# Kernel optimization log

Measured on AMD Instinct MI355X. Metric: run time of the kernel, lower is better.

The kernel has to match this reference:

```python
import jax, jax.numpy as jnp
import numpy as np
from jax import lax

B, T, I, H, L, C = 128, 784, 1, 256, 20, 10  # batch, seq_len, input, hidden, layers, classes


def setup_inputs() -> dict:
    key = jax.random.key(0)
    ks = jax.random.split(key, 9)
    s = 1.0 / np.sqrt(H)  # torch nn.RNN init: U(-1/sqrt(H), 1/sqrt(H))
    u = lambda k, shape: jax.random.uniform(k, shape, jnp.float32, -s, s)
    return {
        "x": jax.random.normal(ks[0], (B, T, I), jnp.float32),
        "W_ih0": u(ks[1], (H, I)),        # layer 0 input proj
        "b_ih0": u(ks[2], (H,)),
        "W_ih": u(ks[3], (L - 1, H, H)),  # layers 1..L-1 input proj
        "b_ih": u(ks[4], (L - 1, H)),
        "W_hh": u(ks[5], (L, H, H)),      # recurrent weights, all layers
        "b_hh": u(ks[6], (L, H)),
        "W_fc": u(ks[7], (C, H)),         # classification head
        "b_fc": u(ks[8], (C,)),
    }


def _rnn_layer(x_seq, W_ih, b_ih, W_hh, b_hh):
    """One vanilla relu-RNN layer. x_seq: [B,T,in] -> [B,T,H]."""
    # Hoist the input projection out of the scan (batched GEMM over all timesteps).
    xp = jnp.einsum('bti,hi->bth', x_seq, W_ih) + b_ih  # [B,T,H]
    h0 = jnp.zeros((x_seq.shape[0], W_hh.shape[0]), x_seq.dtype)

    def step(h, xt):
        h = jax.nn.relu(xt + h @ W_hh.T + b_hh)
        return h, h

    _, ys = lax.scan(step, h0, jnp.swapaxes(xp, 0, 1))  # scan over time
    return jnp.swapaxes(ys, 0, 1)  # [B,T,H]


def reference(x, W_ih0, b_ih0, W_ih, b_ih, W_hh, b_hh, W_fc, b_fc):
    h = _rnn_layer(x, W_ih0, b_ih0, W_hh[0], b_hh[0])
    for l in range(L - 1):  # fixed small layer loop
        h = _rnn_layer(h, W_ih[l], b_ih[l], W_hh[l + 1], b_hh[l + 1])
    last_hidden = h[:, -1, :]  # [B,H]
    return last_hidden @ W_fc.T + b_fc  # [B,C]
```

## Files before the change

### kernel.cpp

```cpp
#include <hip/hip_runtime.h>
#include <hip/hip_fp16.h>


#define B_    128
#define T_    784
#define H_    256
#define L_    20
#define C_    10
#define G_    8
#define BM_   16
#define S_    4
#define NS_   196
#define SW_   280
#define RQWS_ 4096
#define TPB_  512

typedef _Float16 v8h __attribute__((ext_vector_type(8)));
typedef float    v4f __attribute__((ext_vector_type(4)));
typedef unsigned long long u64;

__global__ __launch_bounds__(TPB_, 1)
void rnn_wavefront(const float* __restrict__ x,
                   const float* __restrict__ W_ih0,
                   const float* __restrict__ b_ih0,
                   const float* __restrict__ W_ih,
                   const float* __restrict__ b_ih,
                   const float* __restrict__ W_hh,
                   const float* __restrict__ b_hh,
                   const float* __restrict__ W_fc,
                   const float* __restrict__ b_fc,
                   float* __restrict__ out,
                   unsigned* __restrict__ prod,
                   unsigned* __restrict__ cons,
                   u64* __restrict__ ring,
                   int rmask)
{
    const int l    = blockIdx.x >> 3;
    const int g    = blockIdx.x & 7;
    const int tid  = threadIdx.x;
    const int lane = tid & 63;
    const int wave = tid >> 6;
    const int quad = lane >> 4;
    const int s16  = lane & 15;
    const int nbase = wave * 32;
    const int m_e  = tid >> 5;
    const int n_e  = (tid & 31) * 8;

    __shared__ __align__(16) _Float16 bufX[S_][BM_][SW_];
    __shared__ __align__(16) _Float16 lH[2][BM_][SW_];

    for (int i = tid; i < 2 * BM_ * SW_; i += TPB_) (&lH[0][0][0])[i] = (_Float16)0.f;

    v8h wf[16][2];
#pragma unroll
    for (int kt = 0; kt < 16; ++kt) {
        const int k0 = kt * 32 + quad * 8;
#pragma unroll
        for (int nt = 0; nt < 2; ++nt) {
            const int j = nbase + nt * 16 + s16;
            v8h w;
            if (kt < 8) {
                if (l == 0) {
#pragma unroll
                    for (int i = 0; i < 8; ++i) w[i] = (_Float16)0.f;
                } else {
                    const float* src = &W_ih[(((size_t)(l - 1) * H_) + j) * H_ + k0];
#pragma unroll
                    for (int i = 0; i < 8; ++i) w[i] = (_Float16)src[i];
                }
            } else {
                const float* src = &W_hh[(((size_t)l * H_) + j) * H_ + (k0 - 256)];
#pragma unroll
                for (int i = 0; i < 8; ++i) w[i] = (_Float16)src[i];
            }
            wf[kt][nt] = w;
        }
    }

    float bias[2], w0v[2];
#pragma unroll
    for (int nt = 0; nt < 2; ++nt) {
        const int j = nbase + nt * 16 + s16;
        bias[nt] = b_hh[l * H_ + j] + ((l == 0) ? b_ih0[j] : b_ih[(l - 1) * H_ + j]);
        w0v[nt]  = (l == 0) ? W_ih0[j] : 0.f;
    }

    unsigned* upprod = prod + ((l > 0 ? l - 1 : 0) * G_ + g);
    unsigned* myprod = prod + (l * G_ + g);
    unsigned* mycons = cons + (l * G_ + g);
    unsigned* dncons = cons + (((l < L_ - 1) ? l + 1 : l) * G_ + g);
    const unsigned R = (unsigned)rmask + 1u;
    u64* myring = ring + ((size_t)(l * G_ + g) * (size_t)R) * RQWS_;
    u64* upring = ring + ((size_t)((l > 0 ? l - 1 : 0) * G_ + g) * (size_t)R) * RQWS_;

    unsigned pSeen = 0, cSeen = 0;
    const size_t eidx = (size_t)m_e * 64 + (size_t)(tid & 31) * 2;

    if (l > 0) {
        if (tid == 64) {
            while (pSeen < 2u) {
                pSeen = __hip_atomic_load(upprod, __ATOMIC_RELAXED,
                                          __HIP_MEMORY_SCOPE_AGENT);
                if (pSeen < 2u) __builtin_amdgcn_s_sleep(2);
            }
        }
        __syncthreads();
#pragma unroll
        for (int jj = 0; jj < S_; ++jj) {
            u64 v0 = __hip_atomic_load(upring + (size_t)jj * 1024 + eidx,
                                       __ATOMIC_RELAXED, __HIP_MEMORY_SCOPE_AGENT);
            u64 v1 = __hip_atomic_load(upring + (size_t)jj * 1024 + eidx + 1,
                                       __ATOMIC_RELAXED, __HIP_MEMORY_SCOPE_AGENT);
            *(u64*)&bufX[jj][m_e][n_e]     = v0;
            *(u64*)&bufX[jj][m_e][n_e + 4] = v1;
        }
    }

    for (int s = 0; s < NS_; ++s) {
        const bool pfOK = (l > 0) && (s + 1 < NS_);
        u64 pfv[S_][2];

#pragma unroll
        for (int j = 0; j < S_; ++j) {
            const int t = S_ * s + j;
            __syncthreads();

            if (j == 0) {
                if (tid == 0 && l > 0)
                    __hip_atomic_store(mycons, (unsigned)(s + 1), __ATOMIC_RELAXED,
                                       __HIP_MEMORY_SCOPE_AGENT);
                if (tid == 64 && pfOK) {
                    const unsigned tgt = (unsigned)(s + 2);
                    while (pSeen < tgt) {
                        pSeen = __hip_atomic_load(upprod, __ATOMIC_RELAXED,
                                                  __HIP_MEMORY_SCOPE_AGENT);
                        if (pSeen < tgt) __builtin_amdgcn_s_sleep(2);
                    }
                }
                if (tid == 128 && l < L_ - 1 && s >= (int)R) {
                    const unsigned tgt = (unsigned)(s - (int)R + 1);
                    while (cSeen < tgt) {
                        cSeen = __hip_atomic_load(dncons, __ATOMIC_RELAXED,
                                                  __HIP_MEMORY_SCOPE_AGENT);
                        if (cSeen < tgt) __builtin_amdgcn_s_sleep(2);
                    }
                }
            }

            if (j == 1) {
                if (tid == 0 && l < L_ - 1 && s >= 1)
                    __hip_atomic_store(myprod, (unsigned)s, __ATOMIC_RELAXED,
                                       __HIP_MEMORY_SCOPE_AGENT);
                if (pfOK) {
                    const u64* base = upring + (size_t)((s + 1) & rmask) * RQWS_;
#pragma unroll
                    for (int jj = 0; jj < S_; ++jj) {
                        pfv[jj][0] = __hip_atomic_load(base + (size_t)jj * 1024 + eidx,
                                                       __ATOMIC_RELAXED,
                                                       __HIP_MEMORY_SCOPE_AGENT);
                        pfv[jj][1] = __hip_atomic_load(base + (size_t)jj * 1024 + eidx + 1,
                                                       __ATOMIC_RELAXED,
                                                       __HIP_MEMORY_SCOPE_AGENT);
                    }
                }
            }

            if (l < L_ - 1 && t > 0) {
                u64 e0 = *(const u64*)&lH[t & 1][m_e][n_e];
                u64 e1 = *(const u64*)&lH[t & 1][m_e][n_e + 4];
                u64* d = myring + (size_t)(((t - 1) >> 2) & rmask) * RQWS_
                                + (size_t)((t - 1) & 3) * 1024 + eidx;
                __hip_atomic_store(d,     e0, __ATOMIC_RELAXED, __HIP_MEMORY_SCOPE_AGENT);
                __hip_atomic_store(d + 1, e1, __ATOMIC_RELAXED, __HIP_MEMORY_SCOPE_AGENT);
            }

            v4f acc[2];
            acc[0] = (v4f){0.f, 0.f, 0.f, 0.f};
            acc[1] = (v4f){0.f, 0.f, 0.f, 0.f};
            if (l > 0) {
#pragma unroll
                for (int kt = 0; kt < 8; ++kt) {
                    v8h a = *(const v8h*)&bufX[j][s16][kt * 32 + quad * 8];
                    acc[0] = __builtin_amdgcn_mfma_f32_16x16x32_f16(a, wf[kt][0], acc[0], 0, 0, 0);
                    acc[1] = __builtin_amdgcn_mfma_f32_16x16x32_f16(a, wf[kt][1], acc[1], 0, 0, 0);
                }
            }
#pragma unroll
            for (int kt = 8; kt < 16; ++kt) {
                v8h a = *(const v8h*)&lH[t & 1][s16][(kt - 8) * 32 + quad * 8];
                acc[0] = __builtin_amdgcn_mfma_f32_16x16x32_f16(a, wf[kt][0], acc[0], 0, 0, 0);
                acc[1] = __builtin_amdgcn_mfma_f32_16x16x32_f16(a, wf[kt][1], acc[1], 0, 0, 0);
            }

            float xv[4];
            if (l == 0) {
#pragma unroll
                for (int r = 0; r < 4; ++r)
                    xv[r] = x[(size_t)(g * BM_ + quad * 4 + r) * T_ + t];
            }

#pragma unroll
            for (int nt = 0; nt < 2; ++nt) {
                const int n = nbase + nt * 16 + s16;
#pragma unroll
                for (int r = 0; r < 4; ++r) {
                    float v = acc[nt][r] + bias[nt];
                    if (l == 0) v += xv[r] * w0v[nt];
                    v = fmaxf(v, 0.f);
                    lH[(t + 1) & 1][quad * 4 + r][n] = (_Float16)v;
                }
            }

            if (j == S_ - 1) {
                __syncthreads();
                if (pfOK) {
#pragma unroll
                    for (int jj = 0; jj < S_; ++jj) {
                        *(u64*)&bufX[jj][m_e][n_e]     = pfv[jj][0];
                        *(u64*)&bufX[jj][m_e][n_e + 4] = pfv[jj][1];
                    }
                }
            }
        }
    }

    if (l < L_ - 1) {
        u64 e0 = *(const u64*)&lH[0][m_e][n_e];
        u64 e1 = *(const u64*)&lH[0][m_e][n_e + 4];
        u64* d = myring + (size_t)(((T_ - 1) >> 2) & rmask) * RQWS_
                        + (size_t)3 * 1024 + eidx;
        __hip_atomic_store(d,     e0, __ATOMIC_RELAXED, __HIP_MEMORY_SCOPE_AGENT);
        __hip_atomic_store(d + 1, e1, __ATOMIC_RELAXED, __HIP_MEMORY_SCOPE_AGENT);
        __syncthreads();
        if (tid == 0)
            __hip_atomic_store(myprod, (unsigned)NS_, __ATOMIC_RELAXED,
                               __HIP_MEMORY_SCOPE_AGENT);
    } else {
        __syncthreads();
        if (tid < BM_ * C_) {
            const int bl = tid / C_;
            const int c  = tid % C_;
            float sum = b_fc[c];
            for (int k = 0; k < H_; ++k) sum += (float)lH[0][bl][k] * W_fc[c * H_ + k];
            out[(size_t)(g * BM_ + bl) * C_ + c] = sum;
        }
    }
}

extern "C" void kernel_launch(void* const* d_in, const int* in_sizes, int n_in,
                              void* d_out, int out_size, void* d_ws, size_t ws_size,
                              hipStream_t stream) {
    const float* x     = (const float*)d_in[0];
    const float* W_ih0 = (const float*)d_in[1];
    const float* b_ih0 = (const float*)d_in[2];
    const float* W_ih  = (const float*)d_in[3];
    const float* b_ih  = (const float*)d_in[4];
    const float* W_hh  = (const float*)d_in[5];
    const float* b_hh  = (const float*)d_in[6];
    const float* W_fc  = (const float*)d_in[7];
    const float* b_fc  = (const float*)d_in[8];
    float* out = (float*)d_out;

    const size_t cntBytes = (size_t)L_ * G_ * sizeof(unsigned);
    unsigned* prod = (unsigned*)d_ws;
    unsigned* cons = (unsigned*)((char*)d_ws + cntBytes);
    u64* ring      = (u64*)((char*)d_ws + 2 * cntBytes);

    const size_t slotBytes = (size_t)RQWS_ * 8;
    const size_t base = 2 * cntBytes;
    int R = 4;
    if (ws_size >= base + (size_t)L_ * G_ * 16 * slotBytes) R = 16;
    else if (ws_size >= base + (size_t)L_ * G_ * 8 * slotBytes) R = 8;

    hipMemsetAsync(d_ws, 0, 2 * cntBytes, stream);

    rnn_wavefront<<<dim3(L_ * G_), dim3(TPB_), 0, stream>>>(
        x, W_ih0, b_ih0, W_ih, b_ih, W_hh, b_hh, W_fc, b_fc,
        out, prod, cons, ring, R - 1);
}
```

Baseline: 1.148 ms.

## Remove per-chunk barrier by deferring last prefetch slot and splitting MFMA accumulators

Removes the extra __syncthreads at the end of each 4-step chunk. Prefetched slots 0-2 are written right after their last use, and slot 3 is held in registers until the next chunk begins. The producer/consumer signals are moved to j==0, and the prefetch wait target is raised by one chunk so the longer-lived ring data stays valid. The input-projection and recurrent MFMA chains now use separate accumulators, which shortens the dependent accumulation chain on the per-timestep critical path. In exchange the code holds more registers and has tighter ring-buffer protocol margins.

```diff
diff --git a/kernel.cpp b/kernel.cpp
--- a/kernel.cpp
+++ b/kernel.cpp
@@ -116,6 +116,8 @@
         }
     }
 
+    u64 pfc0 = 0, pfc1 = 0;
+
     for (int s = 0; s < NS_; ++s) {
         const bool pfOK = (l > 0) && (s + 1 < NS_);
         u64 pfv[S_][2];
@@ -126,11 +128,20 @@
             __syncthreads();
 
             if (j == 0) {
-                if (tid == 0 && l > 0)
-                    __hip_atomic_store(mycons, (unsigned)(s + 1), __ATOMIC_RELAXED,
-                                       __HIP_MEMORY_SCOPE_AGENT);
-                if (tid == 64 && pfOK) {
-                    const unsigned tgt = (unsigned)(s + 2);
+                if (l > 0 && s > 0) {
+                    *(u64*)&bufX[3][m_e][n_e]     = pfc0;
+                    *(u64*)&bufX[3][m_e][n_e + 4] = pfc1;
+                }
+                if (tid == 0) {
+                    if (l > 0 && s > 0)
+                        __hip_atomic_store(mycons, (unsigned)s, __ATOMIC_RELAXED,
+                                           __HIP_MEMORY_SCOPE_AGENT);
+                    if (l < L_ - 1 && s >= 1)
+                        __hip_atomic_store(myprod, (unsigned)s, __ATOMIC_RELAXED,
+                                           __HIP_MEMORY_SCOPE_AGENT);
+                }
+                if (tid == 64 && l > 0 && s <= NS_ - 3) {
+                    const unsigned tgt = (unsigned)(s + 3);
                     while (pSeen < tgt) {
                         pSeen = __hip_atomic_load(upprod, __ATOMIC_RELAXED,
                                                   __HIP_MEMORY_SCOPE_AGENT);
@@ -145,12 +156,6 @@
                         if (cSeen < tgt) __builtin_amdgcn_s_sleep(2);
                     }
                 }
-            }
-
-            if (j == 1) {
-                if (tid == 0 && l < L_ - 1 && s >= 1)
-                    __hip_atomic_store(myprod, (unsigned)s, __ATOMIC_RELAXED,
-                                       __HIP_MEMORY_SCOPE_AGENT);
                 if (pfOK) {
                     const u64* base = upring + (size_t)((s + 1) & rmask) * RQWS_;
 #pragma unroll
@@ -174,22 +179,21 @@
                 __hip_atomic_store(d + 1, e1, __ATOMIC_RELAXED, __HIP_MEMORY_SCOPE_AGENT);
             }
 
-            v4f acc[2];
-            acc[0] = (v4f){0.f, 0.f, 0.f, 0.f};
-            acc[1] = (v4f){0.f, 0.f, 0.f, 0.f};
+            v4f accA0 = (v4f){0.f, 0.f, 0.f, 0.f}, accA1 = (v4f){0.f, 0.f, 0.f, 0.f};
+            v4f accB0 = (v4f){0.f, 0.f, 0.f, 0.f}, accB1 = (v4f){0.f, 0.f, 0.f, 0.f};
             if (l > 0) {
 #pragma unroll
                 for (int kt = 0; kt < 8; ++kt) {
                     v8h a = *(const v8h*)&bufX[j][s16][kt * 32 + quad * 8];
-                    acc[0] = __builtin_amdgcn_mfma_f32_16x16x32_f16(a, wf[kt][0], acc[0], 0, 0, 0);
-                    acc[1] = __builtin_amdgcn_mfma_f32_16x16x32_f16(a, wf[kt][1], acc[1], 0, 0, 0);
+                    accA0 = __builtin_amdgcn_mfma_f32_16x16x32_f16(a, wf[kt][0], accA0, 0, 0, 0);
+                    accA1 = __builtin_amdgcn_mfma_f32_16x16x32_f16(a, wf[kt][1], accA1, 0, 0, 0);
                 }
             }
 #pragma unroll
             for (int kt = 8; kt < 16; ++kt) {
                 v8h a = *(const v8h*)&lH[t & 1][s16][(kt - 8) * 32 + quad * 8];
-                acc[0] = __builtin_amdgcn_mfma_f32_16x16x32_f16(a, wf[kt][0], acc[0], 0, 0, 0);
-                acc[1] = __builtin_amdgcn_mfma_f32_16x16x32_f16(a, wf[kt][1], acc[1], 0, 0, 0);
+                accB0 = __builtin_amdgcn_mfma_f32_16x16x32_f16(a, wf[kt][0], accB0, 0, 0, 0);
+                accB1 = __builtin_amdgcn_mfma_f32_16x16x32_f16(a, wf[kt][1], accB1, 0, 0, 0);
             }
 
             float xv[4];
@@ -201,25 +205,26 @@
 
 #pragma unroll
             for (int nt = 0; nt < 2; ++nt) {
+                const v4f aa = nt ? accA1 : accA0;
+                const v4f ab = nt ? accB1 : accB0;
                 const int n = nbase + nt * 16 + s16;
 #pragma unroll
                 for (int r = 0; r < 4; ++r) {
-                    float v = acc[nt][r] + bias[nt];
+                    float v = aa[r] + ab[r] + bias[nt];
                     if (l == 0) v += xv[r] * w0v[nt];
                     v = fmaxf(v, 0.f);
                     lH[(t + 1) & 1][quad * 4 + r][n] = (_Float16)v;
                 }
             }
 
-            if (j == S_ - 1) {
-                __syncthreads();
-                if (pfOK) {
-#pragma unroll
-                    for (int jj = 0; jj < S_; ++jj) {
-                        *(u64*)&bufX[jj][m_e][n_e]     = pfv[jj][0];
-                        *(u64*)&bufX[jj][m_e][n_e + 4] = pfv[jj][1];
-                    }
-                }
+            if (j == S_ - 1 && pfOK) {
+#pragma unroll
+                for (int jj = 0; jj < 3; ++jj) {
+                    *(u64*)&bufX[jj][m_e][n_e]     = pfv[jj][0];
+                    *(u64*)&bufX[jj][m_e][n_e + 4] = pfv[jj][1];
+                }
+                pfc0 = pfv[3][0];
+                pfc1 = pfv[3][1];
             }
         }
     }
```

Result: slower. 1.260 ms (+9.8%).
